# Kernel optimization log

Hardware: AMD Instinct MI355X
Metric: run time of the kernel (lower is better)

Reference implementation:

```python
import jax, jax.numpy as jnp
import numpy as np

H1, H2, H3 = 32, 64, 64
NODEN = 12
NODES_PER_GRAPH = NODEN + 2  # 14
N = 700000                   # 50000 graphs * 14 nodes
E = 4000000


def setup_inputs() -> dict:
    key = jax.random.key(0)
    ks = jax.random.split(key, 8)
    x = jax.random.normal(ks[0], (N, H1), dtype=jnp.float32)
    edges = jax.random.randint(ks[1], (2, E), 0, N, dtype=jnp.int64)
    W1 = jax.random.normal(ks[2], (H1, H2), dtype=jnp.float32) / np.sqrt(H1).astype(np.float32)
    b1 = jnp.zeros((H2,), jnp.float32)
    W2 = jax.random.normal(ks[3], (H2, H3), dtype=jnp.float32) / np.sqrt(H2).astype(np.float32)
    b2 = jnp.zeros((H3,), jnp.float32)
    Wfc = jax.random.normal(ks[4], (H3 * NODES_PER_GRAPH, 1), dtype=jnp.float32) / np.sqrt(H3 * NODES_PER_GRAPH).astype(np.float32)
    bfc = jnp.zeros((1,), jnp.float32)
    return {"x": x, "edges": edges, "W1": W1, "b1": b1, "W2": W2, "b2": b2, "Wfc": Wfc, "bfc": bfc}


def gcn_conv(x, src, dst, W, b, n):
    # PyG GCNConv: h = X W; add self-loops; norm = deg^-1/2[src]*deg^-1/2[dst]
    h = x @ W  # [N, out]
    ones = jnp.ones(src.shape[0], dtype=h.dtype)
    deg = jax.ops.segment_sum(ones, dst, num_segments=n) + jnp.asarray(1.0, h.dtype)  # +1 self-loop
    dinv = jax.lax.rsqrt(deg)  # deg >= 1 always (self-loop)
    norm = dinv[src] * dinv[dst]  # [E]
    agg = jax.ops.segment_sum(h[src] * norm[:, None], dst, num_segments=n)
    agg = agg + h * (dinv * dinv)[:, None]  # self-loop contribution
    return agg + b


def reference(x, edges, W1, b1, W2, b2, Wfc, bfc):
    src, dst = edges[0], edges[1]
    h = jax.nn.relu(gcn_conv(x, src, dst, W1, b1, N))
    # F.dropout(training=False) is identity in eval mode
    h = jax.nn.relu(gcn_conv(h, src, dst, W2, b2, N))
    h = h.reshape(-1, H3 * NODES_PER_GRAPH)  # [B, 896]
    return h @ Wfc + bfc  # [B, 1]
```

## Files before the change

kernel.cpp:

```cpp
#include <hip/hip_runtime.h>
#include <hip/hip_fp16.h>


typedef _Float16 half8 __attribute__((ext_vector_type(8)));
typedef float float4v __attribute__((ext_vector_type(4)));

#define CHUNK 8192
#define BSH 11
#define BNODES 2048
#define DBINS 64

__global__ __launch_bounds__(256) void fallback_kernel(float* __restrict__ out, int n, float v)
{
  int i = blockIdx.x * 256 + threadIdx.x;
  if (i < n) out[i] = v;
}

__global__ __launch_bounds__(64) void probe_kernel(const int* __restrict__ edges, int* __restrict__ flag)
{
  if (threadIdx.x == 0) {
    int orv = edges[1] | edges[3] | edges[5] | edges[7] | edges[9] | edges[11] | edges[13] | edges[15];
    flag[0] = (orv == 0) ? 1 : 0;
  }
}

__global__ __launch_bounds__(64) void zero_dummy_kernel(
    __half* __restrict__ P, __half* __restrict__ F2, int* __restrict__ dhist, int N)
{
  int t = threadIdx.x;
  dhist[t] = 0;
  if (t < 8) ((uint2*)(P + (size_t)N * 32))[t] = make_uint2(0, 0);
  else if (t < 24) ((uint2*)(F2 + (size_t)N * 64))[t - 8] = make_uint2(0, 0);
}

__global__ __launch_bounds__(256) void hist2_kernel(
    const int* __restrict__ edges, int E, int N, const int* __restrict__ flag,
    int* __restrict__ cnt, int NBK)
{
  __shared__ int lh[512];
  int t = threadIdx.x;
  int blk = blockIdx.x;
  for (int b = t; b < NBK; b += 256) lh[b] = 0;
  __syncthreads();
  int sh = flag[0];
  int base = blk * CHUNK;
#pragma unroll
  for (int k = 0; k < CHUNK / 256; k++) {
    int e = base + k * 256 + t;
    if (e < E) {
      int d = edges[(E + e) << sh];
      if ((unsigned)d < (unsigned)N) atomicAdd(&lh[d >> BSH], 1);
    }
  }
  __syncthreads();
  for (int b = t; b < NBK; b += 256) cnt[(size_t)blk * NBK + b] = lh[b];
}

__global__ __launch_bounds__(64) void colscan_kernel(
    int* __restrict__ cnt, int NCH, int NBK, int* __restrict__ totals)
{
  int b = blockIdx.x;
  int lane = threadIdx.x;
  int carry = 0;
  int rounds = (NCH + 63) >> 6;
  for (int r = 0; r < rounds; r++) {
    int blk = r * 64 + lane;
    int v = (blk < NCH) ? cnt[(size_t)blk * NBK + b] : 0;
    int incl = v;
#pragma unroll
    for (int off = 1; off < 64; off <<= 1) {
      int x = __shfl_up(incl, off);
      if (lane >= off) incl += x;
    }
    int excl = incl - v + carry;
    if (blk < NCH) cnt[(size_t)blk * NBK + b] = excl;
    carry += __shfl(incl, 63);
  }
  if (lane == 0) totals[b] = carry;
}

__global__ __launch_bounds__(512) void scan_totals_kernel(
    const int* __restrict__ totals, int NBK,
    int* __restrict__ bstart, int* __restrict__ rowptr, int N)
{
  __shared__ int sm[512];
  int t = threadIdx.x;
  int v = (t < NBK) ? totals[t] : 0;
  sm[t] = v;
  __syncthreads();
  for (int off = 1; off < 512; off <<= 1) {
    int x = 0;
    if (t >= off) x = sm[t - off];
    __syncthreads();
    if (t >= off) sm[t] += x;
    __syncthreads();
  }
  if (t < NBK) bstart[t] = sm[t] - v;
  if (t == 0) { bstart[NBK] = sm[511]; rowptr[N] = sm[511] + N; }
}

__global__ __launch_bounds__(256) void pass3_kernel(
    const int* __restrict__ edges, int E, int N, const int* __restrict__ flag,
    const int* __restrict__ cnt, const int* __restrict__ bstart,
    int* __restrict__ pair, int NBK)
{
  __shared__ int lcur[512];
  int t = threadIdx.x;
  int blk = blockIdx.x;
  for (int b = t; b < NBK; b += 256)
    lcur[b] = bstart[b] + cnt[(size_t)blk * NBK + b];
  __syncthreads();
  int sh = flag[0];
  int base = blk * CHUNK;
#pragma unroll
  for (int k = 0; k < CHUNK / 256; k++) {
    int e = base + k * 256 + t;
    if (e < E) {
      int s = edges[e << sh];
      int d = edges[(E + e) << sh];
      if ((unsigned)s < (unsigned)N && (unsigned)d < (unsigned)N) {
        int pos = atomicAdd(&lcur[d >> BSH], 1);
        pair[pos] = s | ((d & (BNODES - 1)) << 20);
      }
    }
  }
}

__global__ __launch_bounds__(256) void build_kernel(
    const int* __restrict__ pair, const int* __restrict__ bstart,
    int* __restrict__ rowptr, float* __restrict__ dinv, int* __restrict__ col, int N)
{
  __shared__ int hist[BNODES];
  __shared__ int cur[BNODES];
  __shared__ int sc[256];
  int b = blockIdx.x;
  int t = threadIdx.x;
  int pbeg = bstart[b], pend = bstart[b + 1];
  int colbase = pbeg + (b << BSH);
#pragma unroll
  for (int i = 0; i < BNODES / 256; i++) {
    int idx = i * 256 + t;
    int row = (b << BSH) + idx;
    hist[idx] = (row < N) ? 1 : 0;
  }
  __syncthreads();
  for (int p = pbeg + t; p < pend; p += 256)
    atomicAdd(&hist[(pair[p] >> 20) & (BNODES - 1)], 1);
  __syncthreads();
  int hv[8];
  int tsum = 0;
#pragma unroll
  for (int i = 0; i < 8; i++) { hv[i] = hist[t * 8 + i]; tsum += hv[i]; }
  sc[t] = tsum;
  __syncthreads();
  for (int off = 1; off < 256; off <<= 1) {
    int x = 0;
    if (t >= off) x = sc[t - off];
    __syncthreads();
    if (t >= off) sc[t] += x;
    __syncthreads();
  }
  int run = sc[t] - tsum;
#pragma unroll
  for (int i = 0; i < 8; i++) {
    int idx = t * 8 + i;
    int rp = colbase + run;
    int row = (b << BSH) + idx;
    if (row < N) {
      rowptr[row] = rp;
      dinv[row] = rsqrtf((float)hv[i]);
      col[rp] = row;
      cur[idx] = rp + 1;
    } else {
      cur[idx] = rp;
    }
    run += hv[i];
  }
  __syncthreads();
  for (int p = pbeg + t; p < pend; p += 256) {
    int v = pair[p];
    int pos = atomicAdd(&cur[(v >> 20) & (BNODES - 1)], 1);
    col[pos] = v & 0xFFFFF;
  }
}

__global__ __launch_bounds__(256) void deg_hist_kernel(
    const int* __restrict__ rowptr, int* __restrict__ dhist, int N)
{
  __shared__ int lh[DBINS];
  int t = threadIdx.x;
  if (t < DBINS) lh[t] = 0;
  __syncthreads();
  int n = blockIdx.x * 256 + t;
  if (n < N) {
    int rlen = rowptr[n + 1] - rowptr[n];
    int b = rlen < DBINS ? rlen : DBINS - 1;
    atomicAdd(&lh[b], 1);
  }
  __syncthreads();
  if (t < DBINS && lh[t]) atomicAdd(&dhist[t], lh[t]);
}

__global__ __launch_bounds__(64) void deg_scan_kernel(
    const int* __restrict__ dhist, int* __restrict__ dcur)
{
  int t = threadIdx.x;
  int v = dhist[t];
  int incl = v;
#pragma unroll
  for (int off = 1; off < 64; off <<= 1) {
    int x = __shfl_up(incl, off);
    if (t >= off) incl += x;
  }
  dcur[t] = incl - v;
}

__global__ __launch_bounds__(256) void deg_place_kernel(
    const int* __restrict__ rowptr, int* __restrict__ dcur,
    int* __restrict__ perm, int N)
{
  __shared__ int lh[DBINS];
  __shared__ int lbase[DBINS];
  int t = threadIdx.x;
  if (t < DBINS) lh[t] = 0;
  __syncthreads();
  int n = blockIdx.x * 256 + t;
  int b = -1;
  if (n < N) {
    int rlen = rowptr[n + 1] - rowptr[n];
    b = rlen < DBINS ? rlen : DBINS - 1;
    atomicAdd(&lh[b], 1);
  }
  __syncthreads();
  if (t < DBINS) lbase[t] = lh[t] ? atomicAdd(&dcur[t], lh[t]) : 0;
  __syncthreads();
  if (t < DBINS) lh[t] = lbase[t];
  __syncthreads();
  if (n < N) {
    int pos = atomicAdd(&lh[b], 1);
    perm[pos] = n;
  }
}

__global__ __launch_bounds__(256) void scale_x_kernel(
    const float* __restrict__ X, const float* __restrict__ dinv,
    __half* __restrict__ P, int N)
{
  int idx = blockIdx.x * 256 + threadIdx.x;
  int total = N * 4;
  int stride = gridDim.x * 256;
  for (int i = idx; i < total; i += stride) {
    int node = i >> 2, part = i & 3;
    const float4* xp = (const float4*)(X + (size_t)node * 32 + part * 8);
    float dv = dinv[node];
    float4 v0 = xp[0], v1 = xp[1];
    half8 h;
    h[0] = (_Float16)(dv * v0.x); h[1] = (_Float16)(dv * v0.y);
    h[2] = (_Float16)(dv * v0.z); h[3] = (_Float16)(dv * v0.w);
    h[4] = (_Float16)(dv * v1.x); h[5] = (_Float16)(dv * v1.y);
    h[6] = (_Float16)(dv * v1.z); h[7] = (_Float16)(dv * v1.w);
    *(half8*)(P + (size_t)node * 32 + part * 8) = h;
  }
}

__device__ inline void hacc(uint4 v, __half2* a)
{
  a[0] = __hadd2(a[0], *reinterpret_cast<__half2*>(&v.x));
  a[1] = __hadd2(a[1], *reinterpret_cast<__half2*>(&v.y));
  a[2] = __hadd2(a[2], *reinterpret_cast<__half2*>(&v.z));
  a[3] = __hadd2(a[3], *reinterpret_cast<__half2*>(&v.w));
}

__global__ __launch_bounds__(256) void agg1_mfma_kernel(
    const __half* __restrict__ P, const int* __restrict__ rowptr,
    const int* __restrict__ col, const float* __restrict__ dinv,
    const int* __restrict__ perm,
    const float* __restrict__ W1, const float* __restrict__ b1,
    __half* __restrict__ U, int ntiles, int ndummy)
{
  int lane = threadIdx.x & 63;
  int n16 = lane & 15;
  int quad = lane >> 4;

  half8 bf[4];
#pragma unroll
  for (int jb = 0; jb < 4; jb++)
#pragma unroll
    for (int i = 0; i < 8; i++)
      bf[jb][i] = (_Float16)W1[(quad * 8 + i) * 64 + jb * 16 + n16];
  float b1j[4];
#pragma unroll
  for (int jb = 0; jb < 4; jb++) b1j[jb] = b1[jb * 16 + n16];

  const uint4* P4 = (const uint4*)P;
  _Float16* Uh = (_Float16*)U;
  int wave = (blockIdx.x * 256 + threadIdx.x) >> 6;
  int nw = (gridDim.x * 256) >> 6;
  for (int tile = wave; tile < ntiles; tile += nw) {
    int ut = __builtin_amdgcn_readfirstlane(tile);
    int base = ut * 16;
    int node = perm[base + n16];
    int rbeg = rowptr[node];
    int rlen = rowptr[node + 1] - rbeg;

    __half2 z2 = __float2half2_rn(0.f);
    __half2 aA[4] = {z2, z2, z2, z2};
    __half2 aB[4] = {z2, z2, z2, z2};

    for (int j = 0; __any(j < rlen); j += 8) {
      int c[8];
#pragma unroll
      for (int q = 0; q < 8; q++) {
        int cc = col[rbeg + j + q];
        c[q] = (j + q < rlen) ? cc : ndummy;
      }
      uint4 v[8];
#pragma unroll
      for (int q = 0; q < 8; q++) v[q] = P4[((size_t)c[q] << 2) + quad];
#pragma unroll
      for (int q = 0; q < 8; q += 2) { hacc(v[q], aA); hacc(v[q + 1], aB); }
    }
#pragma unroll
    for (int k = 0; k < 4; k++) aA[k] = __hadd2(aA[k], aB[k]);

    half8 a = *reinterpret_cast<half8*>(aA);
    float4v co[4];
#pragma unroll
    for (int jb = 0; jb < 4; jb++) {
      float4v z = {0.f, 0.f, 0.f, 0.f};
      co[jb] = __builtin_amdgcn_mfma_f32_16x16x32_f16(a, bf[jb], z, 0, 0, 0);
    }
#pragma unroll
    for (int r = 0; r < 4; r++) {
      int node2 = __shfl(node, quad * 4 + r);
      float dv = dinv[node2];
#pragma unroll
      for (int jb = 0; jb < 4; jb++) {
        float h = dv * co[jb][r] + b1j[jb];
        h = h > 0.f ? h : 0.f;
        Uh[(size_t)node2 * 64 + jb * 16 + n16] = (_Float16)(dv * h);
      }
    }
  }
}

__global__ __launch_bounds__(256) void out_init_kernel(
    float* __restrict__ out, const float* __restrict__ bfc, int n)
{
  int i = blockIdx.x * 256 + threadIdx.x;
  if (i < n) out[i] = bfc[0];
}

__global__ __launch_bounds__(256) void mfma_final_fused_kernel(
    const __half* __restrict__ U, const int* __restrict__ rowptr,
    const int* __restrict__ col, const float* __restrict__ dinv,
    const int* __restrict__ perm,
    const float* __restrict__ W2, const float* __restrict__ b2,
    const float* __restrict__ Wfc, float* __restrict__ out,
    int ntiles, int ndummy)
{
  int lane = threadIdx.x & 63;
  int n16 = lane & 15;
  int quad = lane >> 4;

  half8 bf[4][2];
#pragma unroll
  for (int jb = 0; jb < 4; jb++)
#pragma unroll
    for (int kf = 0; kf < 2; kf++)
#pragma unroll
      for (int i = 0; i < 8; i++)
        bf[jb][kf][i] = (_Float16)W2[(kf * 32 + quad * 8 + i) * 64 + jb * 16 + n16];
  float b2j[4];
#pragma unroll
  for (int jb = 0; jb < 4; jb++) b2j[jb] = b2[jb * 16 + n16];

  const uint4* U4 = (const uint4*)U;
  int wave = (blockIdx.x * 256 + threadIdx.x) >> 6;
  int nw = (gridDim.x * 256) >> 6;
  for (int tile = wave; tile < ntiles; tile += nw) {
    int ut = __builtin_amdgcn_readfirstlane(tile);
    int base = ut * 16;
    int node = perm[base + n16];
    int rbeg = rowptr[node];
    int rlen = rowptr[node + 1] - rbeg;

    __half2 z2 = __float2half2_rn(0.f);
    __half2 aE0[4] = {z2, z2, z2, z2};
    __half2 aE1[4] = {z2, z2, z2, z2};
    __half2 aO0[4] = {z2, z2, z2, z2};
    __half2 aO1[4] = {z2, z2, z2, z2};

    for (int j = 0; __any(j < rlen); j += 4) {
      int c0 = col[rbeg + j];
      int c1 = col[rbeg + j + 1];
      int c2 = col[rbeg + j + 2];
      int c3 = col[rbeg + j + 3];
      c0 = (j < rlen) ? c0 : ndummy;
      c1 = (j + 1 < rlen) ? c1 : ndummy;
      c2 = (j + 2 < rlen) ? c2 : ndummy;
      c3 = (j + 3 < rlen) ? c3 : ndummy;
      uint4 v00 = U4[((size_t)c0 << 3) + quad];
      uint4 v01 = U4[((size_t)c0 << 3) + 4 + quad];
      uint4 v10 = U4[((size_t)c1 << 3) + quad];
      uint4 v11 = U4[((size_t)c1 << 3) + 4 + quad];
      uint4 v20 = U4[((size_t)c2 << 3) + quad];
      uint4 v21 = U4[((size_t)c2 << 3) + 4 + quad];
      uint4 v30 = U4[((size_t)c3 << 3) + quad];
      uint4 v31 = U4[((size_t)c3 << 3) + 4 + quad];
      hacc(v00, aE0); hacc(v01, aE1);
      hacc(v10, aO0); hacc(v11, aO1);
      hacc(v20, aE0); hacc(v21, aE1);
      hacc(v30, aO0); hacc(v31, aO1);
    }
#pragma unroll
    for (int k = 0; k < 4; k++) {
      aE0[k] = __hadd2(aE0[k], aO0[k]);
      aE1[k] = __hadd2(aE1[k], aO1[k]);
    }
    __half2 dv = __half2half2(__float2half_rn(dinv[node]));
#pragma unroll
    for (int j = 0; j < 4; j++) {
      aE0[j] = __hmul2(aE0[j], dv);
      aE1[j] = __hmul2(aE1[j], dv);
    }
    half8 a0 = *reinterpret_cast<half8*>(aE0);
    half8 a1 = *reinterpret_cast<half8*>(aE1);

    int g_r[4], t_r[4];
#pragma unroll
    for (int r = 0; r < 4; r++) {
      int nd = __shfl(node, quad * 4 + r);
      g_r[r] = nd / 14;
      t_r[r] = nd - g_r[r] * 14;
    }
    float pr[4] = {0.f, 0.f, 0.f, 0.f};
#pragma unroll
    for (int jb = 0; jb < 4; jb++) {
      float4v acc = {0.f, 0.f, 0.f, 0.f};
      acc = __builtin_amdgcn_mfma_f32_16x16x32_f16(a0, bf[jb][0], acc, 0, 0, 0);
      acc = __builtin_amdgcn_mfma_f32_16x16x32_f16(a1, bf[jb][1], acc, 0, 0, 0);
      int j = jb * 16 + n16;
#pragma unroll
      for (int r = 0; r < 4; r++) {
        float h = acc[r] + b2j[jb];
        h = h > 0.f ? h : 0.f;
        pr[r] += h * Wfc[t_r[r] * 64 + j];
      }
    }
#pragma unroll
    for (int r = 0; r < 4; r++) {
#pragma unroll
      for (int off = 1; off < 16; off <<= 1) pr[r] += __shfl_xor(pr[r], off);
    }
    if (n16 == 0) {
#pragma unroll
      for (int r = 0; r < 4; r++) atomicAdd(&out[g_r[r]], pr[r]);
    }
  }
}

extern "C" void kernel_launch(void* const* d_in, const int* in_sizes, int n_in,
                              void* d_out, int out_size, void* d_ws, size_t ws_size,
                              hipStream_t stream)
{
  const float* x = (const float*)d_in[0];
  const int* edges = (const int*)d_in[1];
  const float* W1 = (const float*)d_in[2];
  const float* b1 = (const float*)d_in[3];
  const float* W2 = (const float*)d_in[4];
  const float* b2 = (const float*)d_in[5];
  const float* Wfc = (const float*)d_in[6];
  const float* bfc = (const float*)d_in[7];
  float* out = (float*)d_out;
  (void)n_in;

  const int N = in_sizes[0] / 32;
  const int E = in_sizes[1] / 2;
  const int B = out_size;
  const int NBK = (N + BNODES - 1) >> BSH;
  const int NCH = (E + CHUNK - 1) / CHUNK;
  const int NBLK = (N + 255) / 256;

  char* ws = (char*)d_ws;
  size_t off = 0;
  auto alloc = [&](size_t bytes) -> void* {
    void* p = ws + off;
    off += (bytes + 255) & ~(size_t)255;
    return p;
  };
  int* flag = (int*)alloc(256);
  int* cnt = (int*)alloc((size_t)NCH * NBK * 4);
  int* totals = (int*)alloc((size_t)NBK * 4);
  int* bstart = (int*)alloc(((size_t)NBK + 1) * 4);
  int* col = (int*)alloc(((size_t)E + N + 256) * 4);
  int* rowptr = (int*)alloc(((size_t)N + 1) * 4);
  float* dinv = (float*)alloc((size_t)N * 4);
  int* dhist = (int*)alloc(DBINS * 4);
  int* dcur = (int*)alloc(DBINS * 4);
  int* perm = (int*)alloc((size_t)N * 4);
  __half* P = (__half*)alloc(((size_t)N + 16) * 32 * 2);
  __half* F2 = (__half*)alloc(((size_t)N + 16) * 64 * 2);
  int* pair = (int*)P;

  if (off > ws_size) {
    float v = -(float)(double)(ws_size >> 20);
    fallback_kernel<<<(B + 255) / 256, 256, 0, stream>>>(out, B, v);
    return;
  }

  probe_kernel<<<1, 64, 0, stream>>>(edges, flag);
  zero_dummy_kernel<<<1, 64, 0, stream>>>(P, F2, dhist, N);
  hist2_kernel<<<NCH, 256, 0, stream>>>(edges, E, N, flag, cnt, NBK);
  colscan_kernel<<<NBK, 64, 0, stream>>>(cnt, NCH, NBK, totals);
  scan_totals_kernel<<<1, 512, 0, stream>>>(totals, NBK, bstart, rowptr, N);
  pass3_kernel<<<NCH, 256, 0, stream>>>(edges, E, N, flag, cnt, bstart, pair, NBK);
  build_kernel<<<NBK, 256, 0, stream>>>(pair, bstart, rowptr, dinv, col, N);

  deg_hist_kernel<<<NBLK, 256, 0, stream>>>(rowptr, dhist, N);
  deg_scan_kernel<<<1, 64, 0, stream>>>(dhist, dcur);
  deg_place_kernel<<<NBLK, 256, 0, stream>>>(rowptr, dcur, perm, N);

  int ntiles = (N + 15) / 16;
  scale_x_kernel<<<2048, 256, 0, stream>>>(x, dinv, P, N);
  agg1_mfma_kernel<<<4096, 256, 0, stream>>>(P, rowptr, col, dinv, perm, W1, b1, F2, ntiles, N);
  out_init_kernel<<<(B + 255) / 256, 256, 0, stream>>>(out, bfc, B);
  mfma_final_fused_kernel<<<4096, 256, 0, stream>>>(F2, rowptr, col, dinv, perm, W2, b2, Wfc,
                                                    out, ntiles, N);
}
```

Measured before the change: 592.3 us.

## Relabel nodes into degree-sorted order and store features by position

Nodes are renumbered into their degree-sorted positions. An inverse permutation is built, the CSR column indices are remapped to the new labels, and per-position row info (begin and length) plus dinv are precomputed. The input scaling kernel writes P in permuted order, and both aggregation kernels read rowinfo and dinv directly by tile position. This removes the dependent perm→rowptr→dinv lookup chain, and each tile's outputs land in contiguous rows instead of scattered node rows. In exchange there is an extra kernel that gathers iperm for every edge, plus extra workspace arrays.

```diff
diff --git a/kernel.cpp b/kernel.cpp
--- a/kernel.cpp
+++ b/kernel.cpp
@@ -216,8 +216,9 @@
 }
 
 __global__ __launch_bounds__(256) void deg_place_kernel(
-    const int* __restrict__ rowptr, int* __restrict__ dcur,
-    int* __restrict__ perm, int N)
+    const int* __restrict__ rowptr, const float* __restrict__ dinv, int* __restrict__ dcur,
+    int* __restrict__ perm, int* __restrict__ iperm,
+    int2* __restrict__ rowinfo, float* __restrict__ dinv_p, int N)
 {
   __shared__ int lh[DBINS];
   __shared__ int lbase[DBINS];
@@ -225,9 +226,10 @@
   if (t < DBINS) lh[t] = 0;
   __syncthreads();
   int n = blockIdx.x * 256 + t;
-  int b = -1;
+  int b = -1, rbeg = 0, rlen = 0;
   if (n < N) {
-    int rlen = rowptr[n + 1] - rowptr[n];
+    rbeg = rowptr[n];
+    rlen = rowptr[n + 1] - rbeg;
     b = rlen < DBINS ? rlen : DBINS - 1;
     atomicAdd(&lh[b], 1);
   }
@@ -239,27 +241,41 @@
   if (n < N) {
     int pos = atomicAdd(&lh[b], 1);
     perm[pos] = n;
-  }
-}
-
-__global__ __launch_bounds__(256) void scale_x_kernel(
-    const float* __restrict__ X, const float* __restrict__ dinv,
-    __half* __restrict__ P, int N)
+    iperm[n] = pos;
+    rowinfo[pos] = make_int2(rbeg, rlen);
+    dinv_p[pos] = dinv[n];
+  }
+}
+
+__global__ __launch_bounds__(256) void remap_col_kernel(
+    int* __restrict__ col, const int* __restrict__ iperm,
+    const int* __restrict__ rowptr, int N)
+{
+  int total = rowptr[N];
+  int stride = gridDim.x * 256;
+  for (int k = blockIdx.x * 256 + threadIdx.x; k < total; k += stride)
+    col[k] = iperm[col[k]];
+}
+
+__global__ __launch_bounds__(256) void scale_x_perm_kernel(
+    const float* __restrict__ X, const int* __restrict__ perm,
+    const float* __restrict__ dinv_p, __half* __restrict__ P, int N)
 {
   int idx = blockIdx.x * 256 + threadIdx.x;
   int total = N * 4;
   int stride = gridDim.x * 256;
   for (int i = idx; i < total; i += stride) {
-    int node = i >> 2, part = i & 3;
+    int pos = i >> 2, part = i & 3;
+    int node = perm[pos];
     const float4* xp = (const float4*)(X + (size_t)node * 32 + part * 8);
-    float dv = dinv[node];
+    float dv = dinv_p[pos];
     float4 v0 = xp[0], v1 = xp[1];
     half8 h;
     h[0] = (_Float16)(dv * v0.x); h[1] = (_Float16)(dv * v0.y);
     h[2] = (_Float16)(dv * v0.z); h[3] = (_Float16)(dv * v0.w);
     h[4] = (_Float16)(dv * v1.x); h[5] = (_Float16)(dv * v1.y);
     h[6] = (_Float16)(dv * v1.z); h[7] = (_Float16)(dv * v1.w);
-    *(half8*)(P + (size_t)node * 32 + part * 8) = h;
+    *(half8*)(P + (size_t)pos * 32 + part * 8) = h;
   }
 }
 
@@ -271,10 +287,9 @@
   a[3] = __hadd2(a[3], *reinterpret_cast<__half2*>(&v.w));
 }
 
-__global__ __launch_bounds__(256) void agg1_mfma_kernel(
-    const __half* __restrict__ P, const int* __restrict__ rowptr,
-    const int* __restrict__ col, const float* __restrict__ dinv,
-    const int* __restrict__ perm,
+__global__ __launch_bounds__(256) void agg1_pos_kernel(
+    const __half* __restrict__ P, const int2* __restrict__ rowinfo,
+    const int* __restrict__ col, const float* __restrict__ dinv_p,
     const float* __restrict__ W1, const float* __restrict__ b1,
     __half* __restrict__ U, int ntiles, int ndummy)
 {
@@ -299,9 +314,9 @@
   for (int tile = wave; tile < ntiles; tile += nw) {
     int ut = __builtin_amdgcn_readfirstlane(tile);
     int base = ut * 16;
-    int node = perm[base + n16];
-    int rbeg = rowptr[node];
-    int rlen = rowptr[node + 1] - rbeg;
+    int2 ri = rowinfo[base + n16];
+    int rbeg = ri.x, rlen = ri.y;
+    float dvown = dinv_p[base + n16];
 
     __half2 z2 = __float2half2_rn(0.f);
     __half2 aA[4] = {z2, z2, z2, z2};
@@ -332,13 +347,13 @@
     }
 #pragma unroll
     for (int r = 0; r < 4; r++) {
-      int node2 = __shfl(node, quad * 4 + r);
-      float dv = dinv[node2];
+      int pos2 = base + quad * 4 + r;
+      float dv = __shfl(dvown, quad * 4 + r);
 #pragma unroll
       for (int jb = 0; jb < 4; jb++) {
         float h = dv * co[jb][r] + b1j[jb];
         h = h > 0.f ? h : 0.f;
-        Uh[(size_t)node2 * 64 + jb * 16 + n16] = (_Float16)(dv * h);
+        Uh[(size_t)pos2 * 64 + jb * 16 + n16] = (_Float16)(dv * h);
       }
     }
   }
@@ -352,8 +367,8 @@
 }
 
 __global__ __launch_bounds__(256) void mfma_final_fused_kernel(
-    const __half* __restrict__ U, const int* __restrict__ rowptr,
-    const int* __restrict__ col, const float* __restrict__ dinv,
+    const __half* __restrict__ U, const int2* __restrict__ rowinfo,
+    const int* __restrict__ col, const float* __restrict__ dinv_p,
     const int* __restrict__ perm,
     const float* __restrict__ W2, const float* __restrict__ b2,
     const float* __restrict__ Wfc, float* __restrict__ out,
@@ -381,9 +396,10 @@
   for (int tile = wave; tile < ntiles; tile += nw) {
     int ut = __builtin_amdgcn_readfirstlane(tile);
     int base = ut * 16;
+    int2 ri = rowinfo[base + n16];
+    int rbeg = ri.x, rlen = ri.y;
     int node = perm[base + n16];
-    int rbeg = rowptr[node];
-    int rlen = rowptr[node + 1] - rbeg;
+    float dvown = dinv_p[base + n16];
 
     __half2 z2 = __float2half2_rn(0.f);
     __half2 aE0[4] = {z2, z2, z2, z2};
@@ -418,7 +434,7 @@
       aE0[k] = __hadd2(aE0[k], aO0[k]);
       aE1[k] = __hadd2(aE1[k], aO1[k]);
     }
-    __half2 dv = __half2half2(__float2half_rn(dinv[node]));
+    __half2 dv = __half2half2(__float2half_rn(dvown));
 #pragma unroll
     for (int j = 0; j < 4; j++) {
       aE0[j] = __hmul2(aE0[j], dv);
@@ -499,6 +515,9 @@
   int* dhist = (int*)alloc(DBINS * 4);
   int* dcur = (int*)alloc(DBINS * 4);
   int* perm = (int*)alloc((size_t)N * 4);
+  int* iperm = (int*)alloc((size_t)N * 4);
+  int2* rowinfo = (int2*)alloc((size_t)N * 8);
+  float* dinv_p = (float*)alloc((size_t)N * 4);
   __half* P = (__half*)alloc(((size_t)N + 16) * 32 * 2);
   __half* F2 = (__half*)alloc(((size_t)N + 16) * 64 * 2);
   int* pair = (int*)P;
@@ -519,12 +538,13 @@
 
   deg_hist_kernel<<<NBLK, 256, 0, stream>>>(rowptr, dhist, N);
   deg_scan_kernel<<<1, 64, 0, stream>>>(dhist, dcur);
-  deg_place_kernel<<<NBLK, 256, 0, stream>>>(rowptr, dcur, perm, N);
+  deg_place_kernel<<<NBLK, 256, 0, stream>>>(rowptr, dinv, dcur, perm, iperm, rowinfo, dinv_p, N);
+  remap_col_kernel<<<4096, 256, 0, stream>>>(col, iperm, rowptr, N);
 
   int ntiles = (N + 15) / 16;
-  scale_x_kernel<<<2048, 256, 0, stream>>>(x, dinv, P, N);
-  agg1_mfma_kernel<<<4096, 256, 0, stream>>>(P, rowptr, col, dinv, perm, W1, b1, F2, ntiles, N);
+  scale_x_perm_kernel<<<2048, 256, 0, stream>>>(x, perm, dinv_p, P, N);
+  agg1_pos_kernel<<<4096, 256, 0, stream>>>(P, rowinfo, col, dinv_p, W1, b1, F2, ntiles, N);
   out_init_kernel<<<(B + 255) / 256, 256, 0, stream>>>(out, bfc, B);
-  mfma_final_fused_kernel<<<4096, 256, 0, stream>>>(F2, rowptr, col, dinv, perm, W2, b2, Wfc,
+  mfma_final_fused_kernel<<<4096, 256, 0, stream>>>(F2, rowinfo, col, dinv_p, perm, W2, b2, Wfc,
                                                     out, ntiles, N);
 }
```

Measured after the change: 601.5 us. Within noise of the previous version (+1.5%).
